# Optimization experiments

Hardware: AMD Instinct MI355X
Metric: run time of the kernel (lower is better)

Reference implementation:

```python
import jax, jax.numpy as jnp
import numpy as np

N_NODES = 50000
N_EDGES = 800000
D_IN = 256
D_HID = 256
D_OUT = 256
BN_EPS = 1e-5
NORM_EPS = 1e-12


def _glorot(key, out_dim, in_dim):
    a = np.sqrt(6.0 / (in_dim + out_dim)).astype(np.float32)
    return jax.random.uniform(key, (out_dim, in_dim), jnp.float32, -a, a)


def setup_inputs() -> dict:
    key = jax.random.key(0)
    ks = jax.random.split(key, 8)
    x = jax.random.normal(ks[0], (N_NODES, D_IN), jnp.float32)
    edge_index = jax.random.randint(ks[1], (2, N_EDGES), 0, N_NODES, dtype=jnp.int32)
    batch = jnp.zeros((N_NODES,), jnp.int32)
    return {
        "x": x,
        "W1_l": _glorot(ks[2], D_HID, D_IN),
        "b1_l": jnp.zeros((D_HID,), jnp.float32),
        "W1_r": _glorot(ks[3], D_HID, D_IN),
        "W2_l": _glorot(ks[4], D_OUT, D_HID),
        "b2_l": jnp.zeros((D_OUT,), jnp.float32),
        "W2_r": _glorot(ks[5], D_OUT, D_HID),
        "gamma1": jnp.ones((D_HID,), jnp.float32),
        "beta1": jnp.zeros((D_HID,), jnp.float32),
        "edge_index": edge_index,
        "batch": batch,
    }


def _sage_conv(x, W_l, b_l, W_r, src, dst, n_nodes):
    # PyG SAGEConv (aggr='mean'): out = lin_l(mean_j x_j) + lin_r(x)
    msgs = x[src]                                            # [E, d] gather
    s = jax.ops.segment_sum(msgs, dst, num_segments=n_nodes)  # [N, d] scatter-add
    cnt = jax.ops.segment_sum(jnp.ones((src.shape[0], 1), x.dtype), dst,
                              num_segments=n_nodes)
    agg = jnp.where(cnt > 0, s / jnp.maximum(cnt, 1.0), 0.0)
    return agg @ W_l.T + b_l + x @ W_r.T


def _batch_norm(h, gamma, beta):
    mu = jnp.mean(h, axis=0)
    var = jnp.mean((h - mu) ** 2, axis=0)  # biased, as torch train-mode BN
    return (h - mu) * jax.lax.rsqrt(var + BN_EPS) * gamma + beta


def _l2_normalize(h):
    n = jnp.linalg.norm(h, axis=-1, keepdims=True)
    return h / jnp.maximum(n, NORM_EPS)


def reference(x, W1_l, b1_l, W1_r, W2_l, b2_l, W2_r, gamma1, beta1,
              edge_index, batch):
    n = x.shape[0]
    src, dst = edge_index[0], edge_index[1]
    # layer 1: SAGEConv -> BN (train stats) -> ReLU (dropout = identity in eval)
    h = _sage_conv(x, W1_l, b1_l, W1_r, src, dst, n)
    h = jax.nn.relu(_batch_norm(h, gamma1, beta1))
    # layer 2: SAGEConv -> L2 normalize
    h = _sage_conv(h, W2_l, b2_l, W2_r, src, dst, n)
    node_emb = _l2_normalize(h)
    # global mean pool over batch ids (single graph here), then normalize
    gsum = jax.ops.segment_sum(node_emb, batch, num_segments=1)
    gcnt = jax.ops.segment_sum(jnp.ones((n, 1), node_emb.dtype), batch,
                               num_segments=1)
    graph_emb = _l2_normalize(gsum / jnp.maximum(gcnt, 1.0))
    return node_emb, graph_emb
```

## Files before the change

kernel.cpp:

```cpp
#include <hip/hip_runtime.h>
#include <math.h>

#define NN 50000
#define NE 800000
#define D  256
#define SCB 196

typedef unsigned short u16;
typedef __attribute__((ext_vector_type(8))) short short8;
typedef __attribute__((ext_vector_type(8))) unsigned short u16x8;
typedef __attribute__((ext_vector_type(4))) float f32x4;

__device__ __forceinline__ u16 f2b(float f) {
    unsigned u = __float_as_uint(f);
    return (u16)((u + 0x7FFFu + ((u >> 16) & 1u)) >> 16);
}
__device__ __forceinline__ float b2f(u16 b) {
    return __uint_as_float(((unsigned)b) << 16);
}

__device__ __forceinline__ void gl16(const u16* g, u16* l) {
    __builtin_amdgcn_global_load_lds(
        (const __attribute__((address_space(1))) void*)g,
        (__attribute__((address_space(3))) void*)l, 16, 0, 0);
}

__global__ void degree_kernel(const int* __restrict__ dst, int* __restrict__ deg) {
    int e0 = (blockIdx.x * blockDim.x + threadIdx.x) * 4;
    if (e0 + 3 < NE) {
        int4 d = *(const int4*)&dst[e0];
        atomicAdd(&deg[d.x], 1);
        atomicAdd(&deg[d.y], 1);
        atomicAdd(&deg[d.z], 1);
        atomicAdd(&deg[d.w], 1);
    } else {
        for (int e = e0; e < NE; e++) atomicAdd(&deg[dst[e]], 1);
    }
}

__global__ void scanA_kernel(const int* __restrict__ deg, int* __restrict__ partial) {
    int t = threadIdx.x;
    int i = blockIdx.x * 256 + t;
    int v = (i < NN) ? deg[i] : 0;
#pragma unroll
    for (int o = 32; o; o >>= 1) v += __shfl_xor(v, o);
    __shared__ int sm[4];
    if ((t & 63) == 0) sm[t >> 6] = v;
    __syncthreads();
    if (t == 0) partial[blockIdx.x] = sm[0] + sm[1] + sm[2] + sm[3];
}

__global__ void scanB_kernel(const int* __restrict__ partial, int* __restrict__ base,
                             int* __restrict__ offs) {
    __shared__ int sm[256];
    int t = threadIdx.x;
    int v = (t < SCB) ? partial[t] : 0;
    sm[t] = v;
    __syncthreads();
    for (int off = 1; off < 256; off <<= 1) {
        int u = 0;
        if (t >= off) u = sm[t - off];
        __syncthreads();
        sm[t] += u;
        __syncthreads();
    }
    if (t < SCB) base[t] = sm[t] - v;
    if (t == 255) offs[NN] = sm[255];
}

__global__ void scanC_kernel(const int* __restrict__ deg, const int* __restrict__ base,
                             int* __restrict__ offs, int* __restrict__ cur) {
    __shared__ int sm[256];
    int t = threadIdx.x;
    int i = blockIdx.x * 256 + t;
    int v = (i < NN) ? deg[i] : 0;
    sm[t] = v;
    __syncthreads();
    for (int off = 1; off < 256; off <<= 1) {
        int u = 0;
        if (t >= off) u = sm[t - off];
        __syncthreads();
        sm[t] += u;
        __syncthreads();
    }
    int o = base[blockIdx.x] + sm[t] - v;
    if (i < NN) {
        offs[i] = o;
        cur[i] = o;
    }
}

__global__ void fill_kernel(const int* __restrict__ src, const int* __restrict__ dst,
                            int* __restrict__ cur, int* __restrict__ csr) {
    int e0 = (blockIdx.x * blockDim.x + threadIdx.x) * 4;
    if (e0 + 3 < NE) {
        int4 d = *(const int4*)&dst[e0];
        int4 s = *(const int4*)&src[e0];
        int p0 = atomicAdd(&cur[d.x], 1);
        int p1 = atomicAdd(&cur[d.y], 1);
        int p2 = atomicAdd(&cur[d.z], 1);
        int p3 = atomicAdd(&cur[d.w], 1);
        csr[p0] = s.x;
        csr[p1] = s.y;
        csr[p2] = s.z;
        csr[p3] = s.w;
    } else {
        for (int e = e0; e < NE; e++) {
            int pos = atomicAdd(&cur[dst[e]], 1);
            csr[pos] = src[e];
        }
    }
}

__global__ void wconv_kernel(const float* __restrict__ W1l, const float* __restrict__ W1r,
                             const float* __restrict__ W2l, const float* __restrict__ W2r,
                             u16* __restrict__ Wcat1, u16* __restrict__ Wcat2) {
    int r = blockIdx.x;
    int j = threadIdx.x;
    Wcat1[r * 512 + j]       = f2b(W1l[r * 256 + j]);
    Wcat1[r * 512 + 256 + j] = f2b(W1r[r * 256 + j]);
    Wcat2[r * 512 + j]       = f2b(W2l[r * 256 + j]);
    Wcat2[r * 512 + 256 + j] = f2b(W2r[r * 256 + j]);
}

__global__ void xconv_kernel(const float* __restrict__ x, u16* __restrict__ Acat) {
    int idx = blockIdx.x * blockDim.x + threadIdx.x;
    int r = idx >> 6;
    int c4 = (idx & 63) * 4;
    float4 v = *(const float4*)&x[(size_t)r * 256 + c4];
    ushort4 o;
    o.x = f2b(v.x); o.y = f2b(v.y); o.z = f2b(v.z); o.w = f2b(v.w);
    *(ushort4*)&Acat[(size_t)r * 512 + 256 + c4] = o;
}

__global__ __launch_bounds__(256)
void agg_kernel(const u16* __restrict__ Acat, const int* __restrict__ csr,
                const int* __restrict__ offs, u16* __restrict__ AcatW) {
    int wid = (blockIdx.x * blockDim.x + threadIdx.x) >> 6;
    int lane = threadIdx.x & 63;
    if (wid >= NN) return;
    int beg = offs[wid];
    int end = offs[wid + 1];
    int deg = end - beg;
    int half = lane >> 5;
    int lc = (lane & 31) * 8;
    int mid = beg + ((deg + 1) >> 1);
    int e  = half ? mid : beg;
    int hi = half ? end : mid;
    float a[8] = {0.f, 0.f, 0.f, 0.f, 0.f, 0.f, 0.f, 0.f};
    for (; e + 7 < hi; e += 8) {
        int s0 = csr[e + 0], s1 = csr[e + 1], s2 = csr[e + 2], s3 = csr[e + 3];
        int s4 = csr[e + 4], s5 = csr[e + 5], s6 = csr[e + 6], s7 = csr[e + 7];
        u16x8 v0 = *(const u16x8*)&Acat[(size_t)s0 * 512 + 256 + lc];
        u16x8 v1 = *(const u16x8*)&Acat[(size_t)s1 * 512 + 256 + lc];
        u16x8 v2 = *(const u16x8*)&Acat[(size_t)s2 * 512 + 256 + lc];
        u16x8 v3 = *(const u16x8*)&Acat[(size_t)s3 * 512 + 256 + lc];
        u16x8 v4 = *(const u16x8*)&Acat[(size_t)s4 * 512 + 256 + lc];
        u16x8 v5 = *(const u16x8*)&Acat[(size_t)s5 * 512 + 256 + lc];
        u16x8 v6 = *(const u16x8*)&Acat[(size_t)s6 * 512 + 256 + lc];
        u16x8 v7 = *(const u16x8*)&Acat[(size_t)s7 * 512 + 256 + lc];
#pragma unroll
        for (int i = 0; i < 8; i++)
            a[i] += ((b2f(v0[i]) + b2f(v1[i])) + (b2f(v2[i]) + b2f(v3[i]))) +
                    ((b2f(v4[i]) + b2f(v5[i])) + (b2f(v6[i]) + b2f(v7[i])));
    }
    for (; e + 3 < hi; e += 4) {
        int s0 = csr[e + 0], s1 = csr[e + 1], s2 = csr[e + 2], s3 = csr[e + 3];
        u16x8 v0 = *(const u16x8*)&Acat[(size_t)s0 * 512 + 256 + lc];
        u16x8 v1 = *(const u16x8*)&Acat[(size_t)s1 * 512 + 256 + lc];
        u16x8 v2 = *(const u16x8*)&Acat[(size_t)s2 * 512 + 256 + lc];
        u16x8 v3 = *(const u16x8*)&Acat[(size_t)s3 * 512 + 256 + lc];
#pragma unroll
        for (int i = 0; i < 8; i++)
            a[i] += (b2f(v0[i]) + b2f(v1[i])) + (b2f(v2[i]) + b2f(v3[i]));
    }
    for (; e < hi; e++) {
        int s0 = csr[e];
        u16x8 v0 = *(const u16x8*)&Acat[(size_t)s0 * 512 + 256 + lc];
#pragma unroll
        for (int i = 0; i < 8; i++) a[i] += b2f(v0[i]);
    }
#pragma unroll
    for (int i = 0; i < 8; i++) a[i] += __shfl_xor(a[i], 32);
    float sc = (deg > 0) ? 1.0f / (float)deg : 0.0f;
    if (half == 0) {
        u16x8 o;
#pragma unroll
        for (int i = 0; i < 8; i++) o[i] = f2b(a[i] * sc);
        *(u16x8*)&AcatW[(size_t)wid * 512 + lc] = o;
    }
}

template<int BF16_OUT, int STATS>
__global__ __launch_bounds__(256)
void mfma_gemm_kernel(const u16* __restrict__ A, const u16* __restrict__ W,
                      const float* __restrict__ bias, void* __restrict__ Cout,
                      float* __restrict__ stats) {
    __shared__ u16 As[4][128 * 32];
    __shared__ u16 Bs[4][128 * 32];
    const int tid = threadIdx.x;
    const int l = tid & 63;
    const int wid = tid >> 6;
    const int wr = wid >> 1, wc = wid & 1;
    const int row0 = blockIdx.x * 128;
    const int col0 = blockIdx.y * 128;

    const u16* aptr[2];
    const u16* bptr[2];
#pragma unroll
    for (int i = 0; i < 2; i++) {
        int row = wid * 32 + i * 16 + (l >> 2);
        int kg = (l & 3) ^ ((row >> 1) & 3);
        int ra = row0 + row;
        if (ra > NN - 1) ra = NN - 1;
        aptr[i] = A + (size_t)ra * 512 + kg * 8;
        bptr[i] = W + (size_t)(col0 + row) * 512 + kg * 8;
    }

    f32x4 acc[4][4] = {};

#define STAGE(b, t)                                                          \
    do {                                                                     \
        _Pragma("unroll") for (int i_ = 0; i_ < 2; i_++) {                   \
            u16* al = &As[b][(wid * 32 + i_ * 16) * 32];                     \
            u16* bl = &Bs[b][(wid * 32 + i_ * 16) * 32];                     \
            gl16(aptr[i_] + (t) * 32, al);                                   \
            gl16(bptr[i_] + (t) * 32, bl);                                   \
        }                                                                    \
    } while (0)

    STAGE(0, 0);
    STAGE(1, 1);

    const int kq = l >> 4;
    const int sw = ((l & 15) >> 1) & 3;
#pragma unroll
    for (int t = 0; t < 16; t++) {
        if (t + 2 < 16) STAGE((t + 2) & 3, t + 2);

        if (t < 14)       asm volatile("s_waitcnt vmcnt(8)" ::: "memory");
        else if (t == 14) asm volatile("s_waitcnt vmcnt(4)" ::: "memory");
        else              asm volatile("s_waitcnt vmcnt(0)" ::: "memory");
        __builtin_amdgcn_s_barrier();
        __builtin_amdgcn_sched_barrier(0);

        short8 af[4], bf[4];
#pragma unroll
        for (int m = 0; m < 4; m++) {
            int row = wr * 64 + m * 16 + (l & 15);
            af[m] = *(const short8*)&As[t & 3][row * 32 + (kq ^ sw) * 8];
        }
#pragma unroll
        for (int n = 0; n < 4; n++) {
            int row = wc * 64 + n * 16 + (l & 15);
            bf[n] = *(const short8*)&Bs[t & 3][row * 32 + (kq ^ sw) * 8];
        }
#pragma unroll
        for (int m = 0; m < 4; m++)
#pragma unroll
            for (int n = 0; n < 4; n++)
                acc[m][n] = __builtin_amdgcn_mfma_f32_16x16x32_bf16(
                    af[m], bf[n], acc[m][n], 0, 0, 0);
    }
#undef STAGE

    const int cq = l >> 4;
    const int cc = l & 15;
#pragma unroll
    for (int n = 0; n < 4; n++) {
        int c = col0 + wc * 64 + n * 16 + cc;
        float t0 = 0.f, t1 = 0.f;
#pragma unroll
        for (int m = 0; m < 4; m++) {
#pragma unroll
            for (int j = 0; j < 4; j++) {
                int r = row0 + wr * 64 + m * 16 + cq * 4 + j;
                if (r < NN) {
                    float v = acc[m][n][j] + bias[c];
                    if (BF16_OUT)
                        ((u16*)Cout)[(size_t)r * 256 + c] = f2b(v);
                    else
                        ((float*)Cout)[(size_t)r * 256 + c] = v;
                    if (STATS) { t0 += v; t1 += v * v; }
                }
            }
        }
        if (STATS) {
            t0 += __shfl_xor(t0, 16); t1 += __shfl_xor(t1, 16);
            t0 += __shfl_xor(t0, 32); t1 += __shfl_xor(t1, 32);
            if (cq == 0) {
                atomicAdd(&stats[c], t0);
                atomicAdd(&stats[256 + c], t1);
            }
        }
    }
}

__global__ void bnfin_kernel(const float* __restrict__ stats,
                             const float* __restrict__ gamma,
                             const float* __restrict__ beta,
                             float* __restrict__ scale,
                             float* __restrict__ shift) {
    int j = threadIdx.x;
    const float invN = 1.0f / (float)NN;
    float mu = stats[j] * invN;
    float var = stats[256 + j] * invN - mu * mu;
    float sc = gamma[j] * rsqrtf(var + 1e-5f);
    scale[j] = sc;
    shift[j] = beta[j] - mu * sc;
}

__global__ void bnrelu_kernel(const u16* __restrict__ hb,
                              const float* __restrict__ scale,
                              const float* __restrict__ shift,
                              u16* __restrict__ Acat) {
    int idx = blockIdx.x * blockDim.x + threadIdx.x;
    int r = idx >> 5;
    int c8 = (idx & 31) * 8;
    u16x8 v = *(const u16x8*)&hb[(size_t)r * 256 + c8];
    u16x8 o;
#pragma unroll
    for (int i = 0; i < 8; i++) {
        float f = b2f(v[i]) * scale[c8 + i] + shift[c8 + i];
        o[i] = f2b(fmaxf(f, 0.f));
    }
    *(u16x8*)&Acat[(size_t)r * 512 + 256 + c8] = o;
}

__global__ __launch_bounds__(512)
void l2norm_kernel(float* __restrict__ out, float* __restrict__ gsum) {
    __shared__ float sm[8 * 256];
    int wave = threadIdx.x >> 6;
    int lane = threadIdx.x & 63;
    float c0 = 0.f, c1 = 0.f, c2 = 0.f, c3 = 0.f;
    for (int r = blockIdx.x * 8 + wave; r < NN; r += gridDim.x * 8) {
        float4 v = *(float4*)&out[(size_t)r * 256 + lane * 4];
        float sq = v.x * v.x + v.y * v.y + v.z * v.z + v.w * v.w;
#pragma unroll
        for (int o = 32; o; o >>= 1) sq += __shfl_xor(sq, o);
        float invn = 1.0f / fmaxf(sqrtf(sq), 1e-12f);
        v.x *= invn; v.y *= invn; v.z *= invn; v.w *= invn;
        *(float4*)&out[(size_t)r * 256 + lane * 4] = v;
        c0 += v.x; c1 += v.y; c2 += v.z; c3 += v.w;
    }
    *(float4*)&sm[wave * 256 + lane * 4] = make_float4(c0, c1, c2, c3);
    __syncthreads();
    int t = threadIdx.x;
    if (t < 256) {
        float s = 0.f;
#pragma unroll
        for (int w = 0; w < 8; w++) s += sm[w * 256 + t];
        atomicAdd(&gsum[t], s);
    }
}

__global__ void graph_kernel(const float* __restrict__ gsum, float* __restrict__ gout) {
    __shared__ float wsum[4];
    int j = threadIdx.x;
    float v = gsum[j] * (1.0f / (float)NN);
    float sq = v * v;
#pragma unroll
    for (int o = 32; o; o >>= 1) sq += __shfl_xor(sq, o);
    if ((j & 63) == 0) wsum[j >> 6] = sq;
    __syncthreads();
    float tot = wsum[0] + wsum[1] + wsum[2] + wsum[3];
    gout[j] = v / fmaxf(sqrtf(tot), 1e-12f);
}

extern "C" void kernel_launch(void* const* d_in, const int* in_sizes, int n_in,
                              void* d_out, int out_size, void* d_ws, size_t ws_size,
                              hipStream_t stream) {
    const float* x      = (const float*)d_in[0];
    const float* W1_l   = (const float*)d_in[1];
    const float* b1_l   = (const float*)d_in[2];
    const float* W1_r   = (const float*)d_in[3];
    const float* W2_l   = (const float*)d_in[4];
    const float* b2_l   = (const float*)d_in[5];
    const float* W2_r   = (const float*)d_in[6];
    const float* gamma1 = (const float*)d_in[7];
    const float* beta1  = (const float*)d_in[8];
    const int*   eidx   = (const int*)d_in[9];
    const int* src = eidx;
    const int* dst = eidx + NE;

    char* wsb = (char*)d_ws;
    int*   deg   = (int*)(wsb + 0);
    int*   offs  = (int*)(wsb + 200000);
    int*   cur   = (int*)(wsb + 400004);
    int*   csr   = (int*)(wsb + 600004);
    int*   part  = (int*)(wsb + 3800064);
    int*   base  = (int*)(wsb + 3801088);
    float* stats = (float*)(wsb + 3802112);
    float* gsum  = (float*)(wsb + 3804160);
    float* scale = (float*)(wsb + 3805184);
    float* shift = (float*)(wsb + 3806208);
    u16*   Wcat1 = (u16*)(wsb + 3807232);
    u16*   Wcat2 = (u16*)(wsb + 4069376);
    u16*   hb    = (u16*)(wsb + 4331520);
    u16*   Acat  = (u16*)(wsb + 29931520);
    float* out   = (float*)d_out;
    float* gout  = out + (size_t)NN * 256;

    hipMemsetAsync(deg, 0, NN * sizeof(int), stream);
    hipMemsetAsync(stats, 0, 3072, stream);

    wconv_kernel<<<256, 256, 0, stream>>>(W1_l, W1_r, W2_l, W2_r, Wcat1, Wcat2);
    xconv_kernel<<<12500, 256, 0, stream>>>(x, Acat);

    degree_kernel<<<(NE / 4 + 255) / 256, 256, 0, stream>>>(dst, deg);
    scanA_kernel<<<SCB, 256, 0, stream>>>(deg, part);
    scanB_kernel<<<1, 256, 0, stream>>>(part, base, offs);
    scanC_kernel<<<SCB, 256, 0, stream>>>(deg, base, offs, cur);
    fill_kernel<<<(NE / 4 + 255) / 256, 256, 0, stream>>>(src, dst, cur, csr);

    dim3 ggrid((NN + 127) / 128, 2);

    agg_kernel<<<12500, 256, 0, stream>>>(Acat, csr, offs, Acat);
    mfma_gemm_kernel<1, 1><<<ggrid, 256, 0, stream>>>(Acat, Wcat1, b1_l, hb, stats);
    bnfin_kernel<<<1, 256, 0, stream>>>(stats, gamma1, beta1, scale, shift);
    bnrelu_kernel<<<6250, 256, 0, stream>>>(hb, scale, shift, Acat);

    agg_kernel<<<12500, 256, 0, stream>>>(Acat, csr, offs, Acat);
    mfma_gemm_kernel<0, 0><<<ggrid, 256, 0, stream>>>(Acat, Wcat2, b2_l, out, stats);

    l2norm_kernel<<<1024, 512, 0, stream>>>(out, gsum);
    graph_kernel<<<1, 256, 0, stream>>>(gsum, gout);
}
```

Baseline: 376.9 us.

## Triple-buffer GEMM pipeline and move BN column stats to separate kernel

The GEMM LDS ring shrinks from four stages to three, and each stage is now issued after the barrier with a vmcnt(4) wait. This lowers LDS use per block, which may allow more resident blocks per CU. The BN sum and sum-of-squares accumulation moves out of the GEMM epilogue into a new colstats kernel that rereads the bf16 hidden tensor, and the epilogue loop order is swapped. This removes atomics and shuffles from the GEMM but adds a kernel launch plus an extra pass over the 50000x256 bf16 output. The stats are also now computed from bf16-rounded values.

```diff
diff --git a/kernel.cpp b/kernel.cpp
--- a/kernel.cpp
+++ b/kernel.cpp
@@ -191,13 +191,12 @@
     }
 }
 
-template<int BF16_OUT, int STATS>
+template<int BF16_OUT>
 __global__ __launch_bounds__(256)
 void mfma_gemm_kernel(const u16* __restrict__ A, const u16* __restrict__ W,
-                      const float* __restrict__ bias, void* __restrict__ Cout,
-                      float* __restrict__ stats) {
-    __shared__ u16 As[4][128 * 32];
-    __shared__ u16 Bs[4][128 * 32];
+                      const float* __restrict__ bias, void* __restrict__ Cout) {
+    __shared__ u16 As[3][128 * 32];
+    __shared__ u16 Bs[3][128 * 32];
     const int tid = threadIdx.x;
     const int l = tid & 63;
     const int wid = tid >> 6;
@@ -236,24 +235,23 @@
     const int sw = ((l & 15) >> 1) & 3;
 #pragma unroll
     for (int t = 0; t < 16; t++) {
-        if (t + 2 < 16) STAGE((t + 2) & 3, t + 2);
-
-        if (t < 14)       asm volatile("s_waitcnt vmcnt(8)" ::: "memory");
-        else if (t == 14) asm volatile("s_waitcnt vmcnt(4)" ::: "memory");
-        else              asm volatile("s_waitcnt vmcnt(0)" ::: "memory");
+        if (t < 15) asm volatile("s_waitcnt vmcnt(4)" ::: "memory");
+        else        asm volatile("s_waitcnt vmcnt(0)" ::: "memory");
         __builtin_amdgcn_s_barrier();
         __builtin_amdgcn_sched_barrier(0);
 
+        if (t + 2 < 16) STAGE((t + 2) % 3, t + 2);
+
         short8 af[4], bf[4];
 #pragma unroll
         for (int m = 0; m < 4; m++) {
             int row = wr * 64 + m * 16 + (l & 15);
-            af[m] = *(const short8*)&As[t & 3][row * 32 + (kq ^ sw) * 8];
+            af[m] = *(const short8*)&As[t % 3][row * 32 + (kq ^ sw) * 8];
         }
 #pragma unroll
         for (int n = 0; n < 4; n++) {
             int row = wc * 64 + n * 16 + (l & 15);
-            bf[n] = *(const short8*)&Bs[t & 3][row * 32 + (kq ^ sw) * 8];
+            bf[n] = *(const short8*)&Bs[t % 3][row * 32 + (kq ^ sw) * 8];
         }
 #pragma unroll
         for (int m = 0; m < 4; m++)
@@ -267,11 +265,10 @@
     const int cq = l >> 4;
     const int cc = l & 15;
 #pragma unroll
-    for (int n = 0; n < 4; n++) {
-        int c = col0 + wc * 64 + n * 16 + cc;
-        float t0 = 0.f, t1 = 0.f;
-#pragma unroll
-        for (int m = 0; m < 4; m++) {
+    for (int m = 0; m < 4; m++) {
+#pragma unroll
+        for (int n = 0; n < 4; n++) {
+            int c = col0 + wc * 64 + n * 16 + cc;
 #pragma unroll
             for (int j = 0; j < 4; j++) {
                 int r = row0 + wr * 64 + m * 16 + cq * 4 + j;
@@ -281,19 +278,22 @@
                         ((u16*)Cout)[(size_t)r * 256 + c] = f2b(v);
                     else
                         ((float*)Cout)[(size_t)r * 256 + c] = v;
-                    if (STATS) { t0 += v; t1 += v * v; }
                 }
             }
         }
-        if (STATS) {
-            t0 += __shfl_xor(t0, 16); t1 += __shfl_xor(t1, 16);
-            t0 += __shfl_xor(t0, 32); t1 += __shfl_xor(t1, 32);
-            if (cq == 0) {
-                atomicAdd(&stats[c], t0);
-                atomicAdd(&stats[256 + c], t1);
-            }
-        }
-    }
+    }
+}
+
+__global__ void colstats_kernel(const u16* __restrict__ h, float* __restrict__ stats) {
+    int j = threadIdx.x;
+    float s0 = 0.f, s1 = 0.f;
+    for (int r = blockIdx.x; r < NN; r += gridDim.x) {
+        float v = b2f(h[(size_t)r * 256 + j]);
+        s0 += v;
+        s1 += v * v;
+    }
+    atomicAdd(&stats[j], s0);
+    atomicAdd(&stats[256 + j], s1);
 }
 
 __global__ void bnfin_kernel(const float* __restrict__ stats,
@@ -416,12 +416,13 @@
     dim3 ggrid((NN + 127) / 128, 2);
 
     agg_kernel<<<12500, 256, 0, stream>>>(Acat, csr, offs, Acat);
-    mfma_gemm_kernel<1, 1><<<ggrid, 256, 0, stream>>>(Acat, Wcat1, b1_l, hb, stats);
+    mfma_gemm_kernel<1><<<ggrid, 256, 0, stream>>>(Acat, Wcat1, b1_l, hb);
+    colstats_kernel<<<512, 256, 0, stream>>>(hb, stats);
     bnfin_kernel<<<1, 256, 0, stream>>>(stats, gamma1, beta1, scale, shift);
     bnrelu_kernel<<<6250, 256, 0, stream>>>(hb, scale, shift, Acat);
 
     agg_kernel<<<12500, 256, 0, stream>>>(Acat, csr, offs, Acat);
-    mfma_gemm_kernel<0, 0><<<ggrid, 256, 0, stream>>>(Acat, Wcat2, b2_l, out, stats);
+    mfma_gemm_kernel<0><<<ggrid, 256, 0, stream>>>(Acat, Wcat2, b2_l, out);
 
     l2norm_kernel<<<1024, 512, 0, stream>>>(out, gsum);
     graph_kernel<<<1, 256, 0, stream>>>(gsum, gout);
```

After: 408.7 us. 8.4% more time.
